# Performance work log

Measured on AMD Instinct MI355X. Metric: run time of the kernel, lower is better.

## Reference

```python
import jax, jax.numpy as jnp
import numpy as np

B, NQ, NK = 4, 2048, 2048
DQ, DK, DV, H = 256, 256, 256, 4
DH = DV // H
EPS = 1e-5


def _layernorm(x, g, b):
    m = jnp.mean(x, axis=-1, keepdims=True)
    v = jnp.mean(jnp.square(x - m), axis=-1, keepdims=True)
    return (x - m) * jax.lax.rsqrt(v + EPS) * g + b


def setup_inputs() -> dict:
    key = jax.random.key(0)
    ks = jax.random.split(key, 12)
    s = lambda d: 1.0 / np.sqrt(d)
    return {
        "Q": jax.random.normal(ks[0], (B, NQ, DQ), jnp.float32),
        "K": jax.random.normal(ks[1], (B, NK, DK), jnp.float32),
        "Wq": jax.random.uniform(ks[2], (DQ, DV), jnp.float32, -s(DQ), s(DQ)),
        "bq": jnp.zeros((DV,), jnp.float32),
        "Wk": jax.random.uniform(ks[3], (DK, DV), jnp.float32, -s(DK), s(DK)),
        "bk": jnp.zeros((DV,), jnp.float32),
        "Wv": jax.random.uniform(ks[4], (DK, DV), jnp.float32, -s(DK), s(DK)),
        "bv": jnp.zeros((DV,), jnp.float32),
        "W1": jax.random.uniform(ks[5], (DV, DV), jnp.float32, -s(DV), s(DV)),
        "b1": jnp.zeros((DV,), jnp.float32),
        "W2": jax.random.uniform(ks[6], (DV, DV), jnp.float32, -s(DV), s(DV)),
        "b2": jnp.zeros((DV,), jnp.float32),
        "g0": jnp.ones((DV,), jnp.float32),
        "beta0": jnp.zeros((DV,), jnp.float32),
        "g1": jnp.ones((DV,), jnp.float32),
        "beta1": jnp.zeros((DV,), jnp.float32),
    }


def reference(Q, K, Wq, bq, Wk, bk, Wv, bv, W1, b1, W2, b2, g0, beta0, g1, beta1):
    Qp = (Q @ Wq + bq).reshape(B, NQ, H, DH)  # split last dim into heads
    Kp = (K @ Wk + bk).reshape(B, NK, H, DH)
    Vp = (K @ Wv + bv).reshape(B, NK, H, DH)
    scale = 1.0 / np.sqrt(DH)  # K_.size(-1)**0.5 after head split
    scores = jnp.einsum("bqhd,bkhd->bhqk", Qp, Kp) * scale
    attn = jax.nn.softmax(scores, axis=-1)
    out = jnp.einsum("bhqk,bkhd->bqhd", attn, Vp)
    O = (Qp + out).reshape(B, NQ, DV)  # residual with projected Q, heads re-concat
    O = _layernorm(O, g0, beta0)
    ffn = jax.nn.relu(O @ W1 + b1) @ W2 + b2
    return _layernorm(O + ffn, g1, beta1)
```

## Files before the change

### kernel.cpp

```cpp
#include <hip/hip_runtime.h>


typedef float fx4 __attribute__((ext_vector_type(4)));
typedef short short8 __attribute__((ext_vector_type(8)));
typedef short shortx4 __attribute__((ext_vector_type(4)));
typedef unsigned int uint2v __attribute__((ext_vector_type(2)));
typedef unsigned int uint4v __attribute__((ext_vector_type(4)));

#define BB  4
#define NN  2048
#define DD  256
#define HH  4
#define DHH 64

__device__ __forceinline__ float bf2f(unsigned short u) {
    union { unsigned int i; float f; } v; v.i = ((unsigned int)u) << 16; return v.f;
}
__device__ __forceinline__ unsigned short f2bf(float f) {
    union { float f; unsigned int i; } v; v.f = f;
    unsigned int r = v.i + 0x7FFF + ((v.i >> 16) & 1);
    return (unsigned short)(r >> 16);
}
__device__ __forceinline__ unsigned int fbits(float f) {
    union { float f; unsigned int i; } v; v.f = f; return v.i;
}
__device__ __forceinline__ unsigned int packbf(float lo, float hi) {
    unsigned int a = fbits(lo), b = fbits(hi);
    a = (a + 0x7FFF + ((a >> 16) & 1)) >> 16;
    b = (b + 0x7FFF + ((b >> 16) & 1)) & 0xFFFF0000u;
    return a | b;
}

__global__ __launch_bounds__(256) void wt_prep(
        const float* __restrict__ w0, const float* __restrict__ w1,
        const float* __restrict__ w2, const float* __restrict__ w3,
        const float* __restrict__ w4, unsigned short* __restrict__ dst) {
    __shared__ unsigned short T[64 * 73];
    const int tid = threadIdx.x;
    const int z = blockIdx.z;
    const float* W = (z == 0) ? w0 : (z == 1) ? w1 : (z == 2) ? w2 : (z == 3) ? w3 : w4;
    unsigned short* WT = dst + z * 65536;
    const int nb = blockIdx.x * 64, kb = blockIdx.y * 64;
    {
        int kl = tid >> 2, c0 = (tid & 3) * 16;
        const float* src = W + (size_t)(kb + kl) * DD + nb + c0;
#pragma unroll
        for (int i = 0; i < 16; ++i) T[kl * 73 + c0 + i] = f2bf(src[i]);
    }
    __syncthreads();
    {
        int nl = tid >> 2, k0 = (tid & 3) * 16;
        short8 o0, o1;
#pragma unroll
        for (int i = 0; i < 8; ++i) {
            o0[i] = (short)T[(k0 + i) * 73 + nl];
            o1[i] = (short)T[(k0 + 8 + i) * 73 + nl];
        }
        short8* d = (short8*)(WT + (size_t)(nb + nl) * DD + kb + k0);
        d[0] = o0; d[1] = o1;
    }
}

__global__ __launch_bounds__(256) void vt_prep(
        const unsigned short* __restrict__ Vp, unsigned short* __restrict__ VT2) {
    __shared__ unsigned short T[64 * 73];
    const int tid = threadIdx.x;
    const int hb = blockIdx.y;
    const int b = blockIdx.x >> 5;
    const int keyb = (blockIdx.x & 31) * 64;
    const int bh = b * HH + hb;
    {
        int kl = tid >> 2, c0 = (tid & 3) * 16;
        const short8* src = (const short8*)(Vp + (size_t)(b * NN + keyb + kl) * DD + hb * DHH + c0);
        short8 v0 = src[0], v1 = src[1];
#pragma unroll
        for (int i = 0; i < 8; ++i) {
            T[kl * 73 + c0 + i]     = (unsigned short)v0[i];
            T[kl * 73 + c0 + 8 + i] = (unsigned short)v1[i];
        }
    }
    __syncthreads();
    {
        int dl = tid >> 2, k0 = (tid & 3) * 16;
        short8 o0, o1;
#pragma unroll
        for (int i = 0; i < 8; ++i) {
            o0[i] = (short)T[(k0 + i) * 73 + dl];
            o1[i] = (short)T[(k0 + 8 + i) * 73 + dl];
        }
        const int gkey = keyb + k0;
        const int tl = gkey >> 5;
        const int kin = gkey & 31;
        short8* d = (short8*)(VT2 + ((size_t)(bh * 64 + tl) * 64 + dl) * 32 + kin);
        d[0] = o0; d[1] = o1;
    }
}

__global__ __launch_bounds__(256) void kt_prep(
        const unsigned short* __restrict__ Kp, unsigned short* __restrict__ KT) {
    const int bh = blockIdx.x >> 6;
    const int tl = blockIdx.x & 63;
    const int b = bh >> 2, h = bh & 3;
    const int tid = threadIdx.x;
    const int key = tid >> 3, p = tid & 7;
    short8 v = *(const short8*)(Kp + (size_t)(b * NN + tl * 32 + key) * DD + h * DHH + p * 8);
    unsigned short* dst = KT + (size_t)(bh * 64 + tl) * 2048
                        + (p >> 2) * 1024 + key * 32 + (p & 3) * 8;
    *(short8*)dst = v;
}

template<int AIN, int EP>
__device__ __forceinline__ void gemm32_body(
        const void* __restrict__ Ain, const unsigned short* __restrict__ WT,
        const float* __restrict__ bias, void* __restrict__ Cout, int bx) {
    __shared__ unsigned short As[32 * 264];
    const int tid = threadIdx.x;
    const int lane = tid & 63, w = tid >> 6;
    const int l15 = lane & 15, quad = lane >> 4;
    const int r0 = (bx >> 1) * 32;
    const int c0w = (bx & 1) * 128 + w * 32;
    short8 wf[8][2];
#pragma unroll
    for (int kc = 0; kc < 8; ++kc)
#pragma unroll
        for (int dt = 0; dt < 2; ++dt)
            wf[kc][dt] = *(const short8*)(WT + (size_t)(c0w + dt * 16 + l15) * DD + kc * 32 + 8 * quad);
    float bv[2];
#pragma unroll
    for (int dt = 0; dt < 2; ++dt) bv[dt] = bias[c0w + dt * 16 + l15];
    {
        int row = tid >> 3, c0 = (tid & 7) * 32;
        short8 o[4];
        if (AIN == 0) {
            const fx4* s4 = (const fx4*)((const float*)Ain + (size_t)(r0 + row) * DD + c0);
#pragma unroll
            for (int j = 0; j < 4; ++j) {
                fx4 v0 = s4[2 * j], v1 = s4[2 * j + 1];
#pragma unroll
                for (int i = 0; i < 4; ++i) {
                    o[j][i]     = (short)f2bf(v0[i]);
                    o[j][i + 4] = (short)f2bf(v1[i]);
                }
            }
        } else {
            const short8* s8 = (const short8*)((const unsigned short*)Ain + (size_t)(r0 + row) * DD + c0);
#pragma unroll
            for (int j = 0; j < 4; ++j) o[j] = s8[j];
        }
        short8* d = (short8*)(As + row * 264 + c0);
#pragma unroll
        for (int j = 0; j < 4; ++j) d[j] = o[j];
    }
    __syncthreads();
    fx4 acc[2][2];
#pragma unroll
    for (int mt = 0; mt < 2; ++mt)
#pragma unroll
        for (int dt = 0; dt < 2; ++dt) acc[mt][dt] = (fx4){0.f, 0.f, 0.f, 0.f};
#pragma unroll
    for (int kc = 0; kc < 8; ++kc) {
        short8 a0 = *(const short8*)(As + l15 * 264 + kc * 32 + 8 * quad);
        short8 a1 = *(const short8*)(As + (16 + l15) * 264 + kc * 32 + 8 * quad);
#pragma unroll
        for (int dt = 0; dt < 2; ++dt) {
            acc[0][dt] = __builtin_amdgcn_mfma_f32_16x16x32_bf16(a0, wf[kc][dt], acc[0][dt], 0, 0, 0);
            acc[1][dt] = __builtin_amdgcn_mfma_f32_16x16x32_bf16(a1, wf[kc][dt], acc[1][dt], 0, 0, 0);
        }
    }
#pragma unroll
    for (int mt = 0; mt < 2; ++mt)
#pragma unroll
        for (int r = 0; r < 4; ++r) {
            const size_t grow = r0 + mt * 16 + 4 * quad + r;
#pragma unroll
            for (int dt = 0; dt < 2; ++dt) {
                float v = acc[mt][dt][r] + bv[dt];
                if (EP == 1) v = fmaxf(v, 0.0f);
                ((unsigned short*)Cout)[grow * DD + c0w + dt * 16 + l15] = f2bf(v);
            }
        }
}

__global__ __launch_bounds__(256, 4) void qkv_mfma(
        const float* __restrict__ Q, const float* __restrict__ K,
        const unsigned short* __restrict__ WT5,
        const float* __restrict__ bq, const float* __restrict__ bk,
        const float* __restrict__ bv,
        unsigned short* __restrict__ Qp, unsigned short* __restrict__ Kp,
        unsigned short* __restrict__ Vp) {
    const int z = blockIdx.y;
    const float* A = (z == 0) ? Q : K;
    const float* bias = (z == 0) ? bq : (z == 1) ? bk : bv;
    unsigned short* C = (z == 0) ? Qp : (z == 1) ? Kp : Vp;
    gemm32_body<0, 0>(A, WT5 + z * 65536, bias, C, blockIdx.x);
}

__global__ __launch_bounds__(256, 4) void ffn1_mfma(
        const float* __restrict__ O, const unsigned short* __restrict__ WT1,
        const float* __restrict__ b1, unsigned short* __restrict__ H1) {
    gemm32_body<0, 1>(O, WT1, b1, H1, blockIdx.x);
}

__global__ __launch_bounds__(512, 4) void gemm_ffn2_ln(
        const unsigned short* __restrict__ Ain, const unsigned short* __restrict__ WT,
        const float* __restrict__ bias, const float* __restrict__ R,
        const float* __restrict__ g, const float* __restrict__ be,
        float* __restrict__ out) {
    __shared__ unsigned short As[16 * 264];
    __shared__ float lnb[2][8][16];
    const int tid = threadIdx.x;
    const int lane = tid & 63, w = tid >> 6;
    const int l15 = lane & 15, quad = lane >> 4;
    const int r0 = blockIdx.x * 16;
    const int c0w = w * 32;
    short8 wf[8][2];
#pragma unroll
    for (int kc = 0; kc < 8; ++kc)
#pragma unroll
        for (int dt = 0; dt < 2; ++dt)
            wf[kc][dt] = *(const short8*)(WT + (size_t)(c0w + dt * 16 + l15) * DD + kc * 32 + 8 * quad);
    float bv[2], gv[2], ev[2];
#pragma unroll
    for (int dt = 0; dt < 2; ++dt) {
        int col = c0w + dt * 16 + l15;
        bv[dt] = bias[col]; gv[dt] = g[col]; ev[dt] = be[col];
    }
    {
        int row = tid >> 5, c0 = (tid & 31) * 8;
        *(short8*)(As + row * 264 + c0) = *(const short8*)(Ain + (size_t)(r0 + row) * DD + c0);
    }
    __syncthreads();
    fx4 acc[2];
#pragma unroll
    for (int i = 0; i < 2; ++i) acc[i] = (fx4){0.f, 0.f, 0.f, 0.f};
#pragma unroll
    for (int kc = 0; kc < 8; ++kc) {
        short8 a = *(const short8*)(As + l15 * 264 + kc * 32 + 8 * quad);
#pragma unroll
        for (int dt = 0; dt < 2; ++dt)
            acc[dt] = __builtin_amdgcn_mfma_f32_16x16x32_bf16(a, wf[kc][dt], acc[dt], 0, 0, 0);
    }
    float v[4][2], p1[4], p2[4];
#pragma unroll
    for (int r = 0; r < 4; ++r) {
        p1[r] = 0.f; p2[r] = 0.f;
        const size_t grow = r0 + 4 * quad + r;
#pragma unroll
        for (int dt = 0; dt < 2; ++dt) {
            float x = acc[dt][r] + bv[dt] + R[grow * DD + c0w + dt * 16 + l15];
            v[r][dt] = x; p1[r] += x; p2[r] += x * x;
        }
    }
#pragma unroll
    for (int r = 0; r < 4; ++r) {
#pragma unroll
        for (int off = 1; off <= 8; off <<= 1) {
            p1[r] += __shfl_xor(p1[r], off);
            p2[r] += __shfl_xor(p2[r], off);
        }
    }
    if (l15 == 0) {
#pragma unroll
        for (int r = 0; r < 4; ++r) {
            lnb[0][w][4 * quad + r] = p1[r];
            lnb[1][w][4 * quad + r] = p2[r];
        }
    }
    __syncthreads();
#pragma unroll
    for (int r = 0; r < 4; ++r) {
        const int row = 4 * quad + r;
        float s1 = 0.f, s2 = 0.f;
#pragma unroll
        for (int ww = 0; ww < 8; ++ww) { s1 += lnb[0][ww][row]; s2 += lnb[1][ww][row]; }
        float mean = s1 * (1.0f / 256.0f);
        float var  = s2 * (1.0f / 256.0f) - mean * mean;
        float rstd = rsqrtf(var + 1e-5f);
        const size_t grow = r0 + row;
#pragma unroll
        for (int dt = 0; dt < 2; ++dt)
            out[grow * DD + c0w + dt * 16 + l15] = (v[r][dt] - mean) * rstd * gv[dt] + ev[dt];
    }
}

__global__ __launch_bounds__(256, 2) void attn_mfma(
        const unsigned short* __restrict__ Qp, const unsigned short* __restrict__ KT,
        const unsigned short* __restrict__ VT2, float* __restrict__ Opre) {
    __shared__ unsigned short kbuf[2][2048];
    __shared__ unsigned short vbuf[2][2048];
    __shared__ unsigned int pbuf[4][256];
    const int tid = threadIdx.x;
    const int lane = tid & 63, w = tid >> 6;
    const int l15 = lane & 15, quad = lane >> 4;
    const int gb = blockIdx.x;
    const int bh = ((gb & 7) << 1) | ((gb >> 8) & 1);
    const int qc = (gb >> 3) & 31;
    const int h  = bh & 3;
    const int b  = bh >> 2;
    const int qrow = qc * 64 + w * 16;
    const int sw = 4 * ((l15 >> 1) & 3);

    short8 aq0, aq1;
    {
        const unsigned short* qptr = Qp + ((size_t)(b * NN + qrow + l15) * DD + h * DHH + 8 * quad);
        aq0 = *(const short8*)qptr;
        aq1 = *(const short8*)(qptr + 32);
    }
    fx4 od0 = (fx4){0.f, 0.f, 0.f, 0.f};
    fx4 od1 = (fx4){0.f, 0.f, 0.f, 0.f};
    fx4 od2 = (fx4){0.f, 0.f, 0.f, 0.f};
    fx4 od3 = (fx4){0.f, 0.f, 0.f, 0.f};
    float lsum = 0.0f;

    unsigned int* pw = &pbuf[w][0];
    const int wcol = (2 * quad) ^ sw;
    const int rcol = (4 * quad) ^ sw;
    const unsigned short* ktb = KT  + (size_t)bh * 64 * 2048 + tid * 8;
    const unsigned short* vtb = VT2 + (size_t)bh * 64 * 2048 + tid * 8;
    const int ew = (tid * 8) ^ (((tid >> 3) & 3) << 3);
    const int fo = (l15 * 32 + 8 * quad) ^ (((l15 >> 1) & 3) << 3);

    {
        uint4v kr = *(const uint4v*)ktb;
        uint4v vr = *(const uint4v*)vtb;
        *(uint4v*)&kbuf[0][ew] = kr;
        *(uint4v*)&vbuf[0][ew] = vr;
    }
    __syncthreads();

    for (int t = 0; t < 64; ++t) {
        const int cur = t & 1;
        const int tn = (t < 63) ? t + 1 : 63;
        uint4v kr = *(const uint4v*)(ktb + (size_t)tn * 2048);
        uint4v vr = *(const uint4v*)(vtb + (size_t)tn * 2048);

        const unsigned short* kb = &kbuf[cur][fo];
        short8 ck0 = *(const short8*)(kb);
        short8 ck1 = *(const short8*)(kb + 1024);
        short8 ck2 = *(const short8*)(kb + 512);
        short8 ck3 = *(const short8*)(kb + 1536);
        const unsigned short* vb = &vbuf[cur][fo];
        short8 cv0 = *(const short8*)(vb);
        short8 cv1 = *(const short8*)(vb + 512);
        short8 cv2 = *(const short8*)(vb + 1024);
        short8 cv3 = *(const short8*)(vb + 1536);

        const fx4 z_ = (fx4){0.f, 0.f, 0.f, 0.f};
        fx4 s0 = __builtin_amdgcn_mfma_f32_16x16x32_bf16(ck0, aq0, z_, 0, 0, 0);
        s0     = __builtin_amdgcn_mfma_f32_16x16x32_bf16(ck1, aq1, s0, 0, 0, 0);
        fx4 s1 = __builtin_amdgcn_mfma_f32_16x16x32_bf16(ck2, aq0, z_, 0, 0, 0);
        s1     = __builtin_amdgcn_mfma_f32_16x16x32_bf16(ck3, aq1, s1, 0, 0, 0);
        s0[0] = __expf(s0[0] * 0.125f); s0[1] = __expf(s0[1] * 0.125f);
        s0[2] = __expf(s0[2] * 0.125f); s0[3] = __expf(s0[3] * 0.125f);
        s1[0] = __expf(s1[0] * 0.125f); s1[1] = __expf(s1[1] * 0.125f);
        s1[2] = __expf(s1[2] * 0.125f); s1[3] = __expf(s1[3] * 0.125f);
        lsum += s0[0] + s0[1] + s0[2] + s0[3];
        lsum += s1[0] + s1[1] + s1[2] + s1[3];
        uint2v w1_ = (uint2v){packbf(s0[0], s0[1]), packbf(s0[2], s0[3])};
        uint2v w2_ = (uint2v){packbf(s1[0], s1[1]), packbf(s1[2], s1[3])};
        *(uint2v*)(pw + l15 * 16 + wcol)       = w1_;
        *(uint2v*)(pw + l15 * 16 + (wcol ^ 8)) = w2_;
        short8 bp = *(const short8*)(pw + l15 * 16 + rcol);
        od0 = __builtin_amdgcn_mfma_f32_16x16x32_bf16(cv0, bp, od0, 0, 0, 0);
        od1 = __builtin_amdgcn_mfma_f32_16x16x32_bf16(cv1, bp, od1, 0, 0, 0);
        od2 = __builtin_amdgcn_mfma_f32_16x16x32_bf16(cv2, bp, od2, 0, 0, 0);
        od3 = __builtin_amdgcn_mfma_f32_16x16x32_bf16(cv3, bp, od3, 0, 0, 0);

        *(uint4v*)&kbuf[cur ^ 1][ew] = kr;
        *(uint4v*)&vbuf[cur ^ 1][ew] = vr;
        __syncthreads();
    }

    lsum += __shfl_xor(lsum, 16);
    lsum += __shfl_xor(lsum, 32);
    const float inv = 1.0f / lsum;
    const size_t grow = (size_t)(b * NN) + qrow + l15;
    float* obase = Opre + grow * DD + h * DHH;
    const unsigned short* qpb = Qp + grow * DD + h * DHH;
#define OUT_DT(DT, OD) do {                                                   \
        shortx4 rv_ = *(const shortx4*)(qpb + (DT) * 16 + 4 * quad);          \
        fx4 o_;                                                               \
        o_[0] = OD[0] * inv + bf2f((unsigned short)rv_[0]);                   \
        o_[1] = OD[1] * inv + bf2f((unsigned short)rv_[1]);                   \
        o_[2] = OD[2] * inv + bf2f((unsigned short)rv_[2]);                   \
        o_[3] = OD[3] * inv + bf2f((unsigned short)rv_[3]);                   \
        *(fx4*)(obase + (DT) * 16 + 4 * quad) = o_;                           \
    } while (0)
    OUT_DT(0, od0);
    OUT_DT(1, od1);
    OUT_DT(2, od2);
    OUT_DT(3, od3);
#undef OUT_DT
}

__global__ __launch_bounds__(64) void ln_rows(
        const float* __restrict__ X, const float* __restrict__ g,
        const float* __restrict__ be, float* __restrict__ Y) {
    const int lane = threadIdx.x;
    const size_t row = blockIdx.x;
    fx4 v = ((const fx4*)(X + row * DD))[lane];
    float s1 = v[0]+v[1]+v[2]+v[3];
    float s2 = v[0]*v[0]+v[1]*v[1]+v[2]*v[2]+v[3]*v[3];
#pragma unroll
    for (int off = 32; off >= 1; off >>= 1) {
        s1 += __shfl_xor(s1, off); s2 += __shfl_xor(s2, off);
    }
    float mean = s1 * (1.0f/256.0f);
    float var  = s2 * (1.0f/256.0f) - mean * mean;
    float rstd = rsqrtf(var + 1e-5f);
    fx4 gv = ((const fx4*)g)[lane];
    fx4 ev = ((const fx4*)be)[lane];
    fx4 o;
#pragma unroll
    for (int i = 0; i < 4; ++i) o[i] = (v[i]-mean)*rstd*gv[i] + ev[i];
    ((fx4*)(Y + row * DD))[lane] = o;
}

extern "C" void kernel_launch(void* const* d_in, const int* in_sizes, int n_in,
                              void* d_out, int out_size, void* d_ws, size_t ws_size,
                              hipStream_t stream) {
    (void)in_sizes; (void)n_in; (void)out_size; (void)ws_size;
    const float* Q     = (const float*)d_in[0];
    const float* K     = (const float*)d_in[1];
    const float* Wq    = (const float*)d_in[2];
    const float* bq    = (const float*)d_in[3];
    const float* Wk    = (const float*)d_in[4];
    const float* bk    = (const float*)d_in[5];
    const float* Wv    = (const float*)d_in[6];
    const float* bv    = (const float*)d_in[7];
    const float* W1    = (const float*)d_in[8];
    const float* b1    = (const float*)d_in[9];
    const float* W2    = (const float*)d_in[10];
    const float* b2    = (const float*)d_in[11];
    const float* g0    = (const float*)d_in[12];
    const float* beta0 = (const float*)d_in[13];
    const float* g1    = (const float*)d_in[14];
    const float* beta1 = (const float*)d_in[15];

    char* ws = (char*)d_ws;
    unsigned short* Qp  = (unsigned short*)(ws);
    unsigned short* Kp  = (unsigned short*)(ws + (4u  << 20));
    unsigned short* Vp  = (unsigned short*)(ws + (8u  << 20));
    unsigned short* KT  = Vp;
    unsigned short* VT2 = (unsigned short*)(ws + (12u << 20));
    float*          Opre= (float*)(ws + (16u << 20));
    float*          O   = (float*)(ws + (24u << 20));
    unsigned short* WT5 = (unsigned short*)(ws + (32u << 20));
    unsigned short* H1  = Qp;
    float*          out = (float*)d_out;

    const unsigned short* WT1 = WT5 + 3 * 65536;
    const unsigned short* WT2 = WT5 + 4 * 65536;

    const int M = BB * NN;

    wt_prep<<<dim3(4, 4, 5), 256, 0, stream>>>(Wq, Wk, Wv, W1, W2, WT5);
    qkv_mfma<<<dim3(M / 16, 3), 256, 0, stream>>>(Q, K, WT5, bq, bk, bv, Qp, Kp, Vp);
    vt_prep<<<dim3(128, 4), 256, 0, stream>>>(Vp, VT2);
    kt_prep<<<1024, 256, 0, stream>>>(Kp, KT);
    attn_mfma<<<512, 256, 0, stream>>>(Qp, KT, VT2, Opre);
    ln_rows<<<M, 64, 0, stream>>>(Opre, g0, beta0, O);
    ffn1_mfma<<<M / 16, 256, 0, stream>>>(O, WT1, b1, H1);
    gemm_ffn2_ln<<<M / 16, 512, 0, stream>>>(H1, WT2, b2, O, g1, beta1, out);
}
```

Measured before the change: 193.0 us.

## Split attention over two key halves and merge partials in layernorm kernel

The attention kernel now launches twice as many blocks. Each block handles half of the key sequence and writes unnormalized partial outputs and partial softmax row sums to separate buffers. The first layernorm kernel adds the two partials, divides by the combined sum and adds the projected-Q residual. This is meant to give the GPU more blocks to schedule and shorten each block's serial key loop. The cost is an extra fp32 partial-output buffer written and read, plus some buffer aliasing in the workspace.

Measured after the change: 178.8 us. 1.08x faster.

```diff
diff --git a/kernel.cpp b/kernel.cpp
--- a/kernel.cpp
+++ b/kernel.cpp
@@ -285,7 +285,8 @@
 
 __global__ __launch_bounds__(256, 2) void attn_mfma(
         const unsigned short* __restrict__ Qp, const unsigned short* __restrict__ KT,
-        const unsigned short* __restrict__ VT2, float* __restrict__ Opre) {
+        const unsigned short* __restrict__ VT2, float* __restrict__ Od0,
+        float* __restrict__ Od1, float* __restrict__ Lp) {
     __shared__ unsigned short kbuf[2][2048];
     __shared__ unsigned short vbuf[2][2048];
     __shared__ unsigned int pbuf[4][256];
@@ -293,8 +294,9 @@
     const int lane = tid & 63, w = tid >> 6;
     const int l15 = lane & 15, quad = lane >> 4;
     const int gb = blockIdx.x;
-    const int bh = ((gb & 7) << 1) | ((gb >> 8) & 1);
+    const int bh = ((gb & 7) << 1) | ((gb >> 9) & 1);
     const int qc = (gb >> 3) & 31;
+    const int kh = (gb >> 8) & 1;
     const int h  = bh & 3;
     const int b  = bh >> 2;
     const int qrow = qc * 64 + w * 16;
@@ -315,8 +317,8 @@
     unsigned int* pw = &pbuf[w][0];
     const int wcol = (2 * quad) ^ sw;
     const int rcol = (4 * quad) ^ sw;
-    const unsigned short* ktb = KT  + (size_t)bh * 64 * 2048 + tid * 8;
-    const unsigned short* vtb = VT2 + (size_t)bh * 64 * 2048 + tid * 8;
+    const unsigned short* ktb = KT  + (size_t)(bh * 64 + kh * 32) * 2048 + tid * 8;
+    const unsigned short* vtb = VT2 + (size_t)(bh * 64 + kh * 32) * 2048 + tid * 8;
     const int ew = (tid * 8) ^ (((tid >> 3) & 3) << 3);
     const int fo = (l15 * 32 + 8 * quad) ^ (((l15 >> 1) & 3) << 3);
 
@@ -328,9 +330,9 @@
     }
     __syncthreads();
 
-    for (int t = 0; t < 64; ++t) {
+    for (int t = 0; t < 32; ++t) {
         const int cur = t & 1;
-        const int tn = (t < 63) ? t + 1 : 63;
+        const int tn = (t < 31) ? t + 1 : 31;
         uint4v kr = *(const uint4v*)(ktb + (size_t)tn * 2048);
         uint4v vr = *(const uint4v*)(vtb + (size_t)tn * 2048);
 
@@ -373,32 +375,31 @@
 
     lsum += __shfl_xor(lsum, 16);
     lsum += __shfl_xor(lsum, 32);
-    const float inv = 1.0f / lsum;
     const size_t grow = (size_t)(b * NN) + qrow + l15;
-    float* obase = Opre + grow * DD + h * DHH;
-    const unsigned short* qpb = Qp + grow * DD + h * DHH;
-#define OUT_DT(DT, OD) do {                                                   \
-        shortx4 rv_ = *(const shortx4*)(qpb + (DT) * 16 + 4 * quad);          \
-        fx4 o_;                                                               \
-        o_[0] = OD[0] * inv + bf2f((unsigned short)rv_[0]);                   \
-        o_[1] = OD[1] * inv + bf2f((unsigned short)rv_[1]);                   \
-        o_[2] = OD[2] * inv + bf2f((unsigned short)rv_[2]);                   \
-        o_[3] = OD[3] * inv + bf2f((unsigned short)rv_[3]);                   \
-        *(fx4*)(obase + (DT) * 16 + 4 * quad) = o_;                           \
-    } while (0)
-    OUT_DT(0, od0);
-    OUT_DT(1, od1);
-    OUT_DT(2, od2);
-    OUT_DT(3, od3);
-#undef OUT_DT
+    float* obase = ((kh == 0) ? Od0 : Od1) + grow * DD + h * DHH;
+    *(fx4*)(obase + 0 * 16 + 4 * quad) = od0;
+    *(fx4*)(obase + 1 * 16 + 4 * quad) = od1;
+    *(fx4*)(obase + 2 * 16 + 4 * quad) = od2;
+    *(fx4*)(obase + 3 * 16 + 4 * quad) = od3;
+    if (quad == 0) Lp[(size_t)kh * 32768 + grow * 4 + h] = lsum;
 }
 
 __global__ __launch_bounds__(64) void ln_rows(
-        const float* __restrict__ X, const float* __restrict__ g,
-        const float* __restrict__ be, float* __restrict__ Y) {
+        const float* __restrict__ Od0, const float* __restrict__ Od1,
+        const float* __restrict__ Lp, const unsigned short* __restrict__ Qp,
+        const float* __restrict__ g, const float* __restrict__ be,
+        float* __restrict__ Y) {
     const int lane = threadIdx.x;
     const size_t row = blockIdx.x;
-    fx4 v = ((const fx4*)(X + row * DD))[lane];
+    const int h = lane >> 4;
+    fx4 m0 = ((const fx4*)(Od0 + row * DD))[lane];
+    fx4 m1 = ((const fx4*)(Od1 + row * DD))[lane];
+    const float inv = 1.0f / (Lp[row * 4 + h] + Lp[32768 + row * 4 + h]);
+    shortx4 qv = ((const shortx4*)(Qp + row * DD))[lane];
+    fx4 v;
+#pragma unroll
+    for (int i = 0; i < 4; ++i)
+        v[i] = (m0[i] + m1[i]) * inv + bf2f((unsigned short)qv[i]);
     float s1 = v[0]+v[1]+v[2]+v[3];
     float s2 = v[0]*v[0]+v[1]*v[1]+v[2]*v[2]+v[3]*v[3];
 #pragma unroll
@@ -443,8 +444,10 @@
     unsigned short* Vp  = (unsigned short*)(ws + (8u  << 20));
     unsigned short* KT  = Vp;
     unsigned short* VT2 = (unsigned short*)(ws + (12u << 20));
-    float*          Opre= (float*)(ws + (16u << 20));
-    float*          O   = (float*)(ws + (24u << 20));
+    float*          Od0 = (float*)(ws + (16u << 20));
+    float*          Od1 = (float*)(ws + (24u << 20));
+    float*          O   = Od1;
+    float*          Lp  = (float*)(ws + (4u << 20));
     unsigned short* WT5 = (unsigned short*)(ws + (32u << 20));
     unsigned short* H1  = Qp;
     float*          out = (float*)d_out;
@@ -458,8 +461,8 @@
     qkv_mfma<<<dim3(M / 16, 3), 256, 0, stream>>>(Q, K, WT5, bq, bk, bv, Qp, Kp, Vp);
     vt_prep<<<dim3(128, 4), 256, 0, stream>>>(Vp, VT2);
     kt_prep<<<1024, 256, 0, stream>>>(Kp, KT);
-    attn_mfma<<<512, 256, 0, stream>>>(Qp, KT, VT2, Opre);
-    ln_rows<<<M, 64, 0, stream>>>(Opre, g0, beta0, O);
+    attn_mfma<<<1024, 256, 0, stream>>>(Qp, KT, VT2, Od0, Od1, Lp);
+    ln_rows<<<M, 64, 0, stream>>>(Od0, Od1, Lp, Qp, g0, beta0, O);
     ffn1_mfma<<<M / 16, 256, 0, stream>>>(O, WT1, b1, H1);
     gemm_ffn2_ln<<<M / 16, 512, 0, stream>>>(H1, WT2, b2, O, g1, beta1, out);
 }
```
